# Optimization experiments

Measured on AMD Instinct MI355X. Metric: run time of the kernel, lower is better.

The kernel has to match this reference:

```python
import jax, jax.numpy as jnp
import numpy as np

V = 6          # num_variables
K = 6          # codebook_size
D = 32         # embedding_dim
C = 3          # channels
B = 64         # batch
N = K ** V     # 46656 codebook combinations
EPS = 1e-5     # torch BatchNorm eps
ENTROPY_SCALE = 0.1


def setup_inputs() -> dict:
    key = jax.random.key(0)
    ks = jax.random.split(key, 40)
    i = iter(range(40))
    def rn(shape, s):
        return jax.random.normal(ks[next(i)], shape, dtype=jnp.float32) * s
    def rv(shape):
        return 0.5 + 0.5 * jax.random.uniform(ks[next(i)], shape, dtype=jnp.float32)
    inp = {
        'x': jax.random.normal(ks[next(i)], (B, C, 7, 7), dtype=jnp.float32),
        # encoder
        'conv_w': rn((256, C, 7, 7), 0.08), 'conv_b': rn((256,), 0.01),
        'ebn2_g': 1.0 + rn((256,), 0.1), 'ebn2_b': rn((256,), 0.1),
        'fc1_w': rn((1024, 256), 0.06), 'fc1_b': rn((1024,), 0.01),
        'ebn1_g': 1.0 + rn((1024,), 0.1), 'ebn1_b': rn((1024,), 0.1),
        'fc2_w': rn((V * K, 1024), 0.03), 'fc2_b': rn((V * K,), 0.01),
        # quantizer embeddings (V separate codebooks)
        'embeds': jax.random.normal(ks[next(i)], (V, K, D), dtype=jnp.float32),
        # decoder
        'dfc1_w': rn((1024, V * D), 0.07), 'dfc1_b': rn((1024,), 0.01),
        'dbn1_g': 1.0 + rn((1024,), 0.1), 'dbn1_b': rn((1024,), 0.1),
        'dbn1_rm': rn((1024,), 0.1), 'dbn1_rv': rv((1024,)),
        'dfc2_w': rn((256, 1024), 0.03), 'dfc2_b': rn((256,), 0.01),
        'dbn2_g': 1.0 + rn((256,), 0.1), 'dbn2_b': rn((256,), 0.1),
        'dbn2_rm': rn((256,), 0.1), 'dbn2_rv': rv((256,)),
        'dct1_w': rn((256, 16, 7, 7), 0.05), 'dct1_b': rn((16,), 0.01),
        'dbn3_g': 1.0 + rn((16,), 0.1), 'dbn3_b': rn((16,), 0.1),
        'dbn3_rm': rn((16,), 0.1), 'dbn3_rv': rv((16,)),
        'dct2_w': rn((16, C), 0.2), 'dct2_b': rn((C,), 0.01),
    }
    return inp


def _bn_eval(t, g, b, rm, rvar):
    # eval-mode BatchNorm (running stats); params broadcast over leading dims
    return g * (t - rm) * jax.lax.rsqrt(rvar + EPS) + b


def _bn_train(t, g, b):
    # train-mode BatchNorm1d on (B, F): biased batch statistics over dim 0
    m = t.mean(0)
    v = ((t - m) ** 2).mean(0)
    return g * (t - m) * jax.lax.rsqrt(v + EPS) + b


def _decode_all(embeds, dfc1_w, dfc1_b, dbn1_g, dbn1_b, dbn1_rm, dbn1_rv,
                dfc2_w, dfc2_b, dbn2_g, dbn2_b, dbn2_rm, dbn2_rv,
                dct1_w, dct1_b, dbn3_g, dbn3_b, dbn3_rm, dbn3_rv,
                dct2_w, dct2_b):
    # enumerate all K^V index tuples in itertools.product order (first var slowest)
    idx = jnp.arange(N)
    powers = K ** (V - 1 - jnp.arange(V))
    combos = (idx[:, None] // powers[None, :]) % K          # (N, V)
    z = embeds[jnp.arange(V)[None, :], combos]              # (N, V, D) gather
    h = z.reshape(N, V * D) @ dfc1_w.T + dfc1_b             # (N, 1024)
    h = jax.nn.relu(_bn_eval(h, dbn1_g, dbn1_b, dbn1_rm, dbn1_rv))
    h = h @ dfc2_w.T + dfc2_b                               # (N, 256)
    h = jax.nn.relu(_bn_eval(h, dbn2_g, dbn2_b, dbn2_rm, dbn2_rv))
    # ConvTranspose2d(256,16,7,stride=2) on 1x1 input == einsum with full kernel
    h = jnp.einsum('ni,iohw->nohw', h, dct1_w) + dct1_b[:, None, None]  # (N,16,7,7)
    h = jax.nn.relu(_bn_eval(h, dbn3_g[:, None, None], dbn3_b[:, None, None],
                             dbn3_rm[:, None, None], dbn3_rv[:, None, None]))
    # ConvTranspose2d(16,C,1,1) == pointwise channel mix
    em = jnp.einsum('nihw,io->nohw', h, dct2_w) + dct2_b[:, None, None]  # (N,C,7,7)
    return em


def reference(x, conv_w, conv_b, ebn2_g, ebn2_b, fc1_w, fc1_b, ebn1_g, ebn1_b,
              fc2_w, fc2_b, embeds, dfc1_w, dfc1_b, dbn1_g, dbn1_b, dbn1_rm,
              dbn1_rv, dfc2_w, dfc2_b, dbn2_g, dbn2_b, dbn2_rm, dbn2_rv,
              dct1_w, dct1_b, dbn3_g, dbn3_b, dbn3_rm, dbn3_rv, dct2_w, dct2_b):
    # emission means for every codebook combination (batched decode, BN eval)
    em = _decode_all(embeds, dfc1_w, dfc1_b, dbn1_g, dbn1_b, dbn1_rm, dbn1_rv,
                     dfc2_w, dfc2_b, dbn2_g, dbn2_b, dbn2_rm, dbn2_rv,
                     dct1_w, dct1_b, dbn3_g, dbn3_b, dbn3_rm, dbn3_rv,
                     dct2_w, dct2_b)                         # (N, C, 7, 7)
    # encoder: Conv2d(C,256,7) on 7x7 input collapses to a single GEMM
    e = jnp.einsum('bchw,ochw->bo', x, conv_w) + conv_b      # (B, 256)
    e = jax.nn.relu(_bn_train(e, ebn2_g, ebn2_b))
    e = e @ fc1_w.T + fc1_b                                  # (B, 1024)
    e = jax.nn.relu(_bn_train(e, ebn1_g, ebn1_b))
    logits = e @ fc2_w.T + fc2_b                             # (B, V*K)
    # quantizer
    latent_dist = jax.nn.softmax(logits.reshape(B, V, K), axis=-1)
    latent_loss = ENTROPY_SCALE * jnp.sum(
        latent_dist * jnp.log(latent_dist + 1e-10), axis=(1, 2))
    # obs logits: -0.5 * ||em - x||^2 summed over (C,H,W), via expanded form
    E = em.reshape(N, -1)                                    # (N, 147)
    X = x.reshape(B, -1)                                     # (B, 147)
    obs = -0.5 * (jnp.sum(E * E, -1)[None, :]
                  - 2.0 * (X @ E.T)
                  + jnp.sum(X * X, -1)[:, None])             # (B, N)
    obs_logits = obs.reshape((B,) + (K,) * V)
    return obs_logits, latent_dist, latent_loss
```

## Files before the change

### kernel.cpp

```cpp
#include <hip/hip_runtime.h>
#include <math.h>

#define EPSF 1e-5f
#define NNC 46656

typedef __attribute__((ext_vector_type(4))) float  f32x4;
typedef __attribute__((ext_vector_type(8))) short  short8;
typedef __attribute__((ext_vector_type(8))) unsigned short ushort8;
typedef __attribute__((ext_vector_type(4))) unsigned int uint4v;

__device__ __forceinline__ float bf2f(unsigned short u) {
    unsigned int x = ((unsigned int)u) << 16;
    return __builtin_bit_cast(float, x);
}
__device__ __forceinline__ unsigned short f2bf(float f) {
    unsigned int x = __builtin_bit_cast(unsigned int, f);
    unsigned int r = (x + 0x7fffu + ((x >> 16) & 1u)) >> 16;
    return (unsigned short)r;
}

__device__ __forceinline__ short8 packrelu8(ushort8 H8, ushort8 S8) {
    uint4v H = __builtin_bit_cast(uint4v, H8);
    uint4v S = __builtin_bit_cast(uint4v, S8);
    uint4v O;
#pragma unroll
    for (int d = 0; d < 4; ++d) {
        float hlo = __builtin_bit_cast(float, H[d] << 16);
        float hhi = __builtin_bit_cast(float, H[d] & 0xffff0000u);
        float slo = __builtin_bit_cast(float, S[d] << 16);
        float shi = __builtin_bit_cast(float, S[d] & 0xffff0000u);
        unsigned int rlo = __builtin_bit_cast(unsigned int, fmaxf(hlo + slo, 0.f));
        unsigned int rhi = __builtin_bit_cast(unsigned int, fmaxf(hhi + shi, 0.f));
        O[d] = __builtin_amdgcn_perm(rhi, rlo, 0x07060302u);
    }
    return __builtin_bit_cast(short8, O);
}

#define WS_PP    0u
#define WS_C1    36864u
#define WS_SH    37888u
#define WS_S3    148480u
#define WS_W2BF  259072u
#define WS_C2    390144u
#define WS_W3BF  390400u
#define WS_C3    490752u
#define WS_XBF   490768u
#define WS_SX2   495888u
#define WS_E1T   495952u
#define WS_E2T   512336u

#define OBS_SIZE (64*NNC)
#define DIST_OFF OBS_SIZE
#define LOSS_OFF (OBS_SIZE + 64*36)

#define LDS_BYTES 75008


__global__ void dvae_k1(const float* __restrict__ x,
                        const float* __restrict__ conv_w, const float* __restrict__ conv_b,
                        const float* __restrict__ ebn2_g, const float* __restrict__ ebn2_b,
                        const float* __restrict__ embeds, const float* __restrict__ dfc1_w,
                        const float* __restrict__ dfc1_b,
                        const float* __restrict__ dbn1_g, const float* __restrict__ dbn1_b,
                        const float* __restrict__ dbn1_rm, const float* __restrict__ dbn1_rv,
                        const float* __restrict__ dfc2_w, const float* __restrict__ dfc2_b,
                        const float* __restrict__ dbn2_g, const float* __restrict__ dbn2_b,
                        const float* __restrict__ dbn2_rm, const float* __restrict__ dbn2_rv,
                        const float* __restrict__ dct1_w, const float* __restrict__ dct1_b,
                        const float* __restrict__ dbn3_g, const float* __restrict__ dbn3_b,
                        const float* __restrict__ dbn3_rm, const float* __restrict__ dbn3_rv,
                        float* __restrict__ ws) {
    __shared__ float sbuf[13504];
    int bx = blockIdx.x, tid = threadIdx.x;
    if (bx < 16) {
        float* wtile = sbuf;
        float* semb  = sbuf + 12352;
        int j0 = bx * 64;
        for (int e = tid; e < 64 * 192; e += 256)
            wtile[(e / 192) * 193 + (e % 192)] = dfc1_w[j0 * 192 + e];
        for (int e = tid; e < 1152; e += 256) semb[e] = embeds[e];
        __syncthreads();
        int jL = tid & 63, wvP = tid >> 6;
        int j = j0 + jL;
        float s1 = dbn1_g[j] * rsqrtf(dbn1_rv[j] + EPSF);
#pragma unroll
        for (int vkL = 0; vkL < 9; ++vkL) {
            int vk = wvP * 9 + vkL;
            int v = vk / 6;
            const float* wrow = &wtile[jL * 193 + v * 32];
            const float* ep = &semb[vk * 32];
            float dot = 0.f;
#pragma unroll
            for (int d = 0; d < 32; ++d) dot += wrow[d] * ep[d];
            ws[WS_PP + vk * 1024 + j] = s1 * dot;
        }
        if (tid < 64) {
            int jj = j0 + tid;
            float s = dbn1_g[jj] * rsqrtf(dbn1_rv[jj] + EPSF);
            ws[WS_C1 + jj] = s * dfc1_b[jj] + dbn1_b[jj] - dbn1_rm[jj] * s;
        }
    } else if (bx < 272) {
        int t = (bx - 16) * 256 + tid;
        int i = t >> 8, kq = (t & 255) * 4;
        float s2 = dbn2_g[i] * rsqrtf(dbn2_rv[i] + EPSF);
        float4 w = *(const float4*)(dfc2_w + i * 1024 + kq);
        unsigned short* dst = (unsigned short*)(ws + WS_W2BF) + i * 1024 + kq;
        dst[0] = f2bf(s2 * w.x); dst[1] = f2bf(s2 * w.y);
        dst[2] = f2bf(s2 * w.z); dst[3] = f2bf(s2 * w.w);
        if (kq == 0) ws[WS_C2 + i] = s2 * dfc2_b[i] + dbn2_b[i] - dbn2_rm[i] * s2;
    } else if (bx < 288) {
        int blk = bx - 272;
        for (int e = tid; e < 12544; e += 256) sbuf[e] = dct1_w[blk * 12544 + e];
        __syncthreads();
        unsigned short* W3 = (unsigned short*)(ws + WS_W3BF);
        for (int e = tid; e < 1568; e += 256) {
            int up = e >> 1, k8 = (e & 1) * 8;
            int o = up & 15, hw = up >> 4;
            float s3 = dbn3_g[o] * rsqrtf(dbn3_rv[o] + EPSF);
            ushort8 ov;
#pragma unroll
            for (int t = 0; t < 8; ++t)
                ov[t] = f2bf(s3 * sbuf[(k8 + t) * 784 + o * 49 + hw]);
            *(ushort8*)(W3 + up * 256 + blk * 16 + k8) = ov;
        }
        if (blk == 0 && tid < 16) {
            float s = dbn3_g[tid] * rsqrtf(dbn3_rv[tid] + EPSF);
            ws[WS_C3 + tid] = s * dct1_b[tid] + dbn3_b[tid] - dbn3_rm[tid] * s;
        }
    } else if (bx == 288) {
        unsigned short* Xb = (unsigned short*)(ws + WS_XBF);
        if (tid < 64) {
            const float* xp = x + tid * 147;
            float s = 0.f;
            for (int qq = 0; qq < 147; ++qq) { float v = xp[qq]; s += v * v; }
            ws[WS_SX2 + tid] = s;
        }
        for (int e = tid; e < 64 * 160; e += 256) {
            int b = e / 160, col = e % 160;
            float v = 0.f;
            if (col < 147) { int hw = col / 3, c = col % 3; v = x[b * 147 + c * 49 + hw]; }
            Xb[e] = f2bf(v);
        }
    } else {
        int blk = bx - 289;
        for (int e = tid; e < 9408; e += 256) sbuf[e] = x[e];
        __syncthreads();
        int b = tid & 63;
        int oL = __builtin_amdgcn_readfirstlane(tid >> 6);
        int o = blk * 4 + oL;
        const float* wp = conv_w + o * 147;
        float acc = conv_b[o];
        for (int qq = 0; qq < 147; ++qq) acc += sbuf[b * 147 + qq] * wp[qq];
        float m = acc;
#pragma unroll
        for (int s = 1; s < 64; s <<= 1) m += __shfl_xor(m, s);
        m *= (1.f / 64.f);
        float d = acc - m;
        float var = d * d;
#pragma unroll
        for (int s = 1; s < 64; s <<= 1) var += __shfl_xor(var, s);
        var *= (1.f / 64.f);
        float y = ebn2_g[o] * d * rsqrtf(var + EPSF) + ebn2_b[o];
        ws[WS_E1T + o * 64 + b] = fmaxf(y, 0.f);
    }
}


__global__ void dvae_k2(const float* __restrict__ fc1_w, const float* __restrict__ fc1_b,
                        const float* __restrict__ ebn1_g, const float* __restrict__ ebn1_b,
                        float* __restrict__ ws) {
    int bx = blockIdx.x, tid = threadIdx.x;
    const float* Pp = ws + WS_PP;
    if (bx < 108) {
        int t = bx * 256 + tid;
        int gh = t >> 7, kg = (t & 127) * 8;
        int d0 = gh / 36, d1 = (gh / 6) % 6, d2 = gh % 6;
        const float* r0 = Pp + d0 * 1024 + kg;
        const float* r1 = Pp + (6 + d1) * 1024 + kg;
        const float* r2 = Pp + (12 + d2) * 1024 + kg;
        const float* cc = ws + WS_C1 + kg;
        ushort8 o;
#pragma unroll
        for (int e = 0; e < 8; ++e) o[e] = f2bf(cc[e] + r0[e] + r1[e] + r2[e]);
        *(ushort8*)((unsigned short*)(ws + WS_SH) + gh * 1024 + kg) = o;
    } else if (bx < 216) {
        int t = (bx - 108) * 256 + tid;
        int gl = t >> 7, kg = (t & 127) * 8;
        int d3 = gl / 36, d4 = (gl / 6) % 6, d5 = gl % 6;
        const float* r3 = Pp + (18 + d3) * 1024 + kg;
        const float* r4 = Pp + (24 + d4) * 1024 + kg;
        const float* r5 = Pp + (30 + d5) * 1024 + kg;
        ushort8 o;
#pragma unroll
        for (int e = 0; e < 8; ++e) o[e] = f2bf(r3[e] + r4[e] + r5[e]);
        *(ushort8*)((unsigned short*)(ws + WS_S3) + gl * 1024 + kg) = o;
    } else {
        int blk = bx - 216;
        int b = tid & 63;
        int jL = __builtin_amdgcn_readfirstlane(tid >> 6);
        int j = blk * 4 + jL;
        const float* e1 = ws + WS_E1T;
        const float* wp = fc1_w + j * 256;
        float acc = fc1_b[j];
        for (int o = 0; o < 256; ++o) acc += e1[o * 64 + b] * wp[o];
        float m = acc;
#pragma unroll
        for (int s = 1; s < 64; s <<= 1) m += __shfl_xor(m, s);
        m *= (1.f / 64.f);
        float d = acc - m;
        float var = d * d;
#pragma unroll
        for (int s = 1; s < 64; s <<= 1) var += __shfl_xor(var, s);
        var *= (1.f / 64.f);
        float y = ebn1_g[j] * d * rsqrtf(var + EPSF) + ebn1_b[j];
        ws[WS_E2T + j * 64 + b] = fmaxf(y, 0.f);
    }
}


__launch_bounds__(256, 2)
__global__ void dvae_k3(const unsigned short* __restrict__ Sh,
                        const unsigned short* __restrict__ S3g,
                        const unsigned short* __restrict__ W2,
                        const float* __restrict__ c2g,
                        const unsigned short* __restrict__ W3,
                        const float* __restrict__ c3g,
                        const float* __restrict__ d2wg,
                        const float* __restrict__ d2bg,
                        const unsigned short* __restrict__ Xg,
                        const float* __restrict__ sx2g,
                        const float* __restrict__ e2T,
                        const float* __restrict__ fc2_w,
                        const float* __restrict__ fc2_b,
                        float* __restrict__ out) {
    extern __shared__ char sm[];
    int tid = threadIdx.x;

    if (blockIdx.x == 0) {
        float* wch = (float*)sm;
        float* ech = (float*)(sm + 18432);
        float* LG  = (float*)(sm + 51200);
        int b = tid & 63;
        int wvU = __builtin_amdgcn_readfirstlane(tid >> 6);
        float accv[9];
#pragma unroll
        for (int it = 0; it < 9; ++it) accv[it] = 0.f;
        for (int ch = 0; ch < 8; ++ch) {
            __syncthreads();
            for (int e = tid; e < 36 * 128; e += 256) {
                int o = e >> 7, jl = e & 127;
                wch[e] = fc2_w[o * 1024 + ch * 128 + jl];
            }
            for (int e = tid; e < 128 * 64; e += 256)
                ech[e] = e2T[(ch * 128 + (e >> 6)) * 64 + (e & 63)];
            __syncthreads();
            for (int jl = 0; jl < 128; ++jl) {
                float ev = ech[jl * 64 + b];
#pragma unroll
                for (int it = 0; it < 9; ++it)
                    accv[it] += ev * wch[(wvU + it * 4) * 128 + jl];
            }
        }
#pragma unroll
        for (int it = 0; it < 9; ++it) {
            int o = wvU + it * 4;
            LG[b * 36 + o] = accv[it] + fc2_b[o];
        }
        __syncthreads();
        if (tid < 64) {
            float loss = 0.f;
#pragma unroll
            for (int v = 0; v < 6; ++v) {
                float mx = -1e30f;
#pragma unroll
                for (int k = 0; k < 6; ++k) mx = fmaxf(mx, LG[tid * 36 + v * 6 + k]);
                float s = 0.f, ex[6];
#pragma unroll
                for (int k = 0; k < 6; ++k) { ex[k] = expf(LG[tid * 36 + v * 6 + k] - mx); s += ex[k]; }
                float inv = 1.f / s;
#pragma unroll
                for (int k = 0; k < 6; ++k) {
                    float dd = ex[k] * inv;
                    out[DIST_OFF + tid * 36 + v * 6 + k] = dd;
                    loss += dd * logf(dd + 1e-10f);
                }
            }
            out[LOSS_OFF + tid] = 0.1f * loss;
        }
        return;
    }

    int wv = tid >> 6, lane = tid & 63, l15 = lane & 15, q = lane >> 4;
    int nbase = (blockIdx.x - 1) * 64;
    float* sE2p = (float*)(sm + 0);
    float* sE2f = (float*)(sm + 1024);
    unsigned short* emL = (unsigned short*)(sm + 1280);
    float* h3w = (float*)(sm + 21760 + wv * 5120);
    unsigned short* h2L = (unsigned short*)(sm + 42240);

    f32x4 acc[4][4];
#pragma unroll
    for (int a = 0; a < 4; ++a)
#pragma unroll
        for (int b = 0; b < 4; ++b) acc[a][b] = (f32x4){0.f, 0.f, 0.f, 0.f};

    const unsigned short* pSh[4];
    const unsigned short* pS3[4];
#pragma unroll
    for (int mt = 0; mt < 4; ++mt) {
        int nm = nbase + mt * 16 + l15;
        int gh = nm / 216;
        int r216 = nm - gh * 216;
        pSh[mt] = Sh + gh * 1024 + q * 8;
        pS3[mt] = S3g + r216 * 1024 + q * 8;
    }
    const unsigned short* bbase = W2 + (wv * 64 + l15) * 1024 + q * 8;

    ushort8 sa[4], sb[4];
    short8 bpre[4];
#pragma unroll
    for (int mt = 0; mt < 4; ++mt) { sa[mt] = *(const ushort8*)(pSh[mt]); sb[mt] = *(const ushort8*)(pS3[mt]); }
#pragma unroll
    for (int j = 0; j < 4; ++j) bpre[j] = *(const short8*)(bbase + j * 16384);

#pragma unroll 2
    for (int s = 0; s < 32; ++s) {
        short8 af[4];
#pragma unroll
        for (int mt = 0; mt < 4; ++mt) af[mt] = packrelu8(sa[mt], sb[mt]);
        short8 bcur[4];
#pragma unroll
        for (int j = 0; j < 4; ++j) bcur[j] = bpre[j];
        if (s < 31) {
            int off = (s + 1) * 32;
#pragma unroll
            for (int mt = 0; mt < 4; ++mt) {
                sa[mt] = *(const ushort8*)(pSh[mt] + off);
                sb[mt] = *(const ushort8*)(pS3[mt] + off);
            }
#pragma unroll
            for (int j = 0; j < 4; ++j) bpre[j] = *(const short8*)(bbase + j * 16384 + off);
        }
#pragma unroll
        for (int mt = 0; mt < 4; ++mt)
#pragma unroll
            for (int j = 0; j < 4; ++j)
                acc[mt][j] = __builtin_amdgcn_mfma_f32_16x16x32_bf16(af[mt], bcur[j], acc[mt][j], 0, 0, 0);
    }
#pragma unroll
    for (int j = 0; j < 4; ++j) {
        int i = wv * 64 + j * 16 + l15;
        float cc = c2g[i];
#pragma unroll
        for (int mt = 0; mt < 4; ++mt)
#pragma unroll
            for (int r = 0; r < 4; ++r) {
                int m = mt * 16 + q * 4 + r;
                h2L[((i >> 3) * 64 + m) * 8 + (i & 7)] = f2bf(fmaxf(acc[mt][j][r] + cc, 0.f));
            }
    }
    __syncthreads();

    float c3v = c3g[l15];
    float db0 = d2bg[0], db1 = d2bg[1], db2 = d2bg[2];
    float dw0[16], dw1[16], dw2[16];
#pragma unroll
    for (int o = 0; o < 16; ++o) {
        dw0[o] = d2wg[o * 3 + 0]; dw1[o] = d2wg[o * 3 + 1]; dw2[o] = d2wg[o * 3 + 2];
    }
    float sE2a = 0.f;
    for (int c = wv; c < 13; c += 4) {
        int hw0 = c * 4;
        f32x4 a2[4][4];
#pragma unroll
        for (int a = 0; a < 4; ++a)
#pragma unroll
            for (int b = 0; b < 4; ++b) a2[a][b] = (f32x4){0.f, 0.f, 0.f, 0.f};
        const unsigned short* b3[4];
#pragma unroll
        for (int j = 0; j < 4; ++j) {
            int hw = hw0 + j; if (hw > 48) hw = 48;
            b3[j] = W3 + (hw * 16 + l15) * 256 + q * 8;
        }
        short8 bpre2[4];
#pragma unroll
        for (int j = 0; j < 4; ++j) bpre2[j] = *(const short8*)(b3[j]);
#pragma unroll
        for (int s = 0; s < 8; ++s) {
            short8 bcur[4];
#pragma unroll
            for (int j = 0; j < 4; ++j) bcur[j] = bpre2[j];
            if (s < 7) {
#pragma unroll
                for (int j = 0; j < 4; ++j) bpre2[j] = *(const short8*)(b3[j] + (s + 1) * 32);
            }
            short8 af[4];
#pragma unroll
            for (int mt = 0; mt < 4; ++mt)
                af[mt] = *(const short8*)(h2L + ((s * 4 + q) * 64 + mt * 16 + l15) * 8);
#pragma unroll
            for (int mt = 0; mt < 4; ++mt)
#pragma unroll
                for (int j = 0; j < 4; ++j)
                    a2[mt][j] = __builtin_amdgcn_mfma_f32_16x16x32_bf16(af[mt], bcur[j], a2[mt][j], 0, 0, 0);
        }
#pragma unroll
        for (int j = 0; j < 4; ++j) {
            int hw = hw0 + j;
            if (hw <= 48) {
#pragma unroll
                for (int mt = 0; mt < 4; ++mt)
#pragma unroll
                    for (int r = 0; r < 4; ++r)
                        h3w[(mt * 16 + q * 4 + r) * 20 + l15] = fmaxf(a2[mt][j][r] + c3v, 0.f);
                float hvv[16];
#pragma unroll
                for (int g = 0; g < 4; ++g) {
                    f32x4 tv = *(const f32x4*)(h3w + lane * 20 + g * 4);
                    hvv[g * 4 + 0] = tv[0]; hvv[g * 4 + 1] = tv[1];
                    hvv[g * 4 + 2] = tv[2]; hvv[g * 4 + 3] = tv[3];
                }
                float e0 = db0, e1 = db1, e2 = db2;
#pragma unroll
                for (int o = 0; o < 16; ++o) {
                    e0 += hvv[o] * dw0[o]; e1 += hvv[o] * dw1[o]; e2 += hvv[o] * dw2[o];
                }
                unsigned short u0 = f2bf(e0), u1 = f2bf(e1), u2 = f2bf(e2);
                float f0 = bf2f(u0), f1 = bf2f(u1), f2v = bf2f(u2);
                sE2a += f0 * f0 + f1 * f1 + f2v * f2v;
                emL[lane * 160 + hw * 3 + 0] = u0;
                emL[lane * 160 + hw * 3 + 1] = u1;
                emL[lane * 160 + hw * 3 + 2] = u2;
            }
        }
    }
    sE2p[wv * 64 + lane] = sE2a;
    for (int e = tid; e < 64 * 13; e += 256) emL[(e / 13) * 160 + 147 + (e % 13)] = 0;
    __syncthreads();
    if (tid < 64) sE2f[tid] = sE2p[tid] + sE2p[64 + tid] + sE2p[128 + tid] + sE2p[192 + tid];
    __syncthreads();

    f32x4 aO[4];
#pragma unroll
    for (int j = 0; j < 4; ++j) aO[j] = (f32x4){0.f, 0.f, 0.f, 0.f};
    const unsigned short* xrow = Xg + (wv * 16 + l15) * 160 + q * 8;
#pragma unroll
    for (int s = 0; s < 5; ++s) {
        short8 af = *(const short8*)(xrow + s * 32);
#pragma unroll
        for (int j = 0; j < 4; ++j) {
            short8 bfv = *(const short8*)(emL + (j * 16 + l15) * 160 + s * 32 + q * 8);
            aO[j] = __builtin_amdgcn_mfma_f32_16x16x32_bf16(af, bfv, aO[j], 0, 0, 0);
        }
    }
    int b0 = wv * 16 + q * 4;
    float sxv[4];
#pragma unroll
    for (int r = 0; r < 4; ++r) sxv[r] = sx2g[b0 + r];
#pragma unroll
    for (int j = 0; j < 4; ++j) {
        int n = nbase + j * 16 + l15;
        float he = 0.5f * sE2f[j * 16 + l15];
#pragma unroll
        for (int r = 0; r < 4; ++r)
            out[(size_t)(b0 + r) * NNC + n] = aO[j][r] - he - 0.5f * sxv[r];
    }
}


extern "C" void kernel_launch(void* const* d_in, const int* in_sizes, int n_in,
                              void* d_out, int out_size, void* d_ws, size_t ws_size,
                              hipStream_t stream) {
    const float* x       = (const float*)d_in[0];
    const float* conv_w  = (const float*)d_in[1];
    const float* conv_b  = (const float*)d_in[2];
    const float* ebn2_g  = (const float*)d_in[3];
    const float* ebn2_b  = (const float*)d_in[4];
    const float* fc1_w   = (const float*)d_in[5];
    const float* fc1_b   = (const float*)d_in[6];
    const float* ebn1_g  = (const float*)d_in[7];
    const float* ebn1_b  = (const float*)d_in[8];
    const float* fc2_w   = (const float*)d_in[9];
    const float* fc2_b   = (const float*)d_in[10];
    const float* embeds  = (const float*)d_in[11];
    const float* dfc1_w  = (const float*)d_in[12];
    const float* dfc1_b  = (const float*)d_in[13];
    const float* dbn1_g  = (const float*)d_in[14];
    const float* dbn1_b  = (const float*)d_in[15];
    const float* dbn1_rm = (const float*)d_in[16];
    const float* dbn1_rv = (const float*)d_in[17];
    const float* dfc2_w  = (const float*)d_in[18];
    const float* dfc2_b  = (const float*)d_in[19];
    const float* dbn2_g  = (const float*)d_in[20];
    const float* dbn2_b  = (const float*)d_in[21];
    const float* dbn2_rm = (const float*)d_in[22];
    const float* dbn2_rv = (const float*)d_in[23];
    const float* dct1_w  = (const float*)d_in[24];
    const float* dct1_b  = (const float*)d_in[25];
    const float* dbn3_g  = (const float*)d_in[26];
    const float* dbn3_b  = (const float*)d_in[27];
    const float* dbn3_rm = (const float*)d_in[28];
    const float* dbn3_rv = (const float*)d_in[29];
    const float* dct2_w  = (const float*)d_in[30];
    const float* dct2_b  = (const float*)d_in[31];

    float* ws  = (float*)d_ws;
    float* out = (float*)d_out;

    dvae_k1<<<353, 256, 0, stream>>>(x, conv_w, conv_b, ebn2_g, ebn2_b,
                                     embeds, dfc1_w, dfc1_b, dbn1_g, dbn1_b, dbn1_rm, dbn1_rv,
                                     dfc2_w, dfc2_b, dbn2_g, dbn2_b, dbn2_rm, dbn2_rv,
                                     dct1_w, dct1_b, dbn3_g, dbn3_b, dbn3_rm, dbn3_rv, ws);
    dvae_k2<<<472, 256, 0, stream>>>(fc1_w, fc1_b, ebn1_g, ebn1_b, ws);

    hipFuncSetAttribute(reinterpret_cast<const void*>(dvae_k3),
                        hipFuncAttributeMaxDynamicSharedMemorySize, LDS_BYTES);
    dvae_k3<<<730, 256, LDS_BYTES, stream>>>(
        (const unsigned short*)(ws + WS_SH), (const unsigned short*)(ws + WS_S3),
        (const unsigned short*)(ws + WS_W2BF), ws + WS_C2,
        (const unsigned short*)(ws + WS_W3BF), ws + WS_C3,
        dct2_w, dct2_b,
        (const unsigned short*)(ws + WS_XBF), ws + WS_SX2,
        ws + WS_E2T, fc2_w, fc2_b, out);
}
```

Before: 279.1 us.

## Halve k3 codebook tile to 32 rows to raise occupancy and block count

The main decoder/obs kernel now processes 32 codebook combinations per block instead of 64. This halves LDS use and accumulator registers, raises launch bounds to 4 blocks per SIMD set, and doubles the grid to about 1459 blocks for better latency hiding and load balance. In exchange, the fc2 weight B-fragments are reused over fewer rows, so W2/W3 global loads per output double, and half the lanes sit idle in the decode epilogue. The first kernel's dfc1 projection is also split across 64 smaller blocks, and two scalar loops get unroll pragmas.

```diff
diff --git a/kernel.cpp b/kernel.cpp
--- a/kernel.cpp
+++ b/kernel.cpp
@@ -53,7 +53,7 @@
 #define DIST_OFF OBS_SIZE
 #define LOSS_OFF (OBS_SIZE + 64*36)
 
-#define LDS_BYTES 75008
+#define LDS_BYTES 37504
 
 
 __global__ void dvae_k1(const float* __restrict__ x,
@@ -70,22 +70,20 @@
                         const float* __restrict__ dbn3_g, const float* __restrict__ dbn3_b,
                         const float* __restrict__ dbn3_rm, const float* __restrict__ dbn3_rv,
                         float* __restrict__ ws) {
-    __shared__ float sbuf[13504];
+    __shared__ float sbuf[12544];
     int bx = blockIdx.x, tid = threadIdx.x;
-    if (bx < 16) {
+    if (bx < 64) {
         float* wtile = sbuf;
-        float* semb  = sbuf + 12352;
-        int j0 = bx * 64;
-        for (int e = tid; e < 64 * 192; e += 256)
+        float* semb  = sbuf + 3088;
+        int j0 = bx * 16;
+        for (int e = tid; e < 16 * 192; e += 256)
             wtile[(e / 192) * 193 + (e % 192)] = dfc1_w[j0 * 192 + e];
         for (int e = tid; e < 1152; e += 256) semb[e] = embeds[e];
         __syncthreads();
-        int jL = tid & 63, wvP = tid >> 6;
+        int jL = tid & 15, vk0 = tid >> 4;
         int j = j0 + jL;
         float s1 = dbn1_g[j] * rsqrtf(dbn1_rv[j] + EPSF);
-#pragma unroll
-        for (int vkL = 0; vkL < 9; ++vkL) {
-            int vk = wvP * 9 + vkL;
+        for (int vk = vk0; vk < 36; vk += 16) {
             int v = vk / 6;
             const float* wrow = &wtile[jL * 193 + v * 32];
             const float* ep = &semb[vk * 32];
@@ -94,13 +92,13 @@
             for (int d = 0; d < 32; ++d) dot += wrow[d] * ep[d];
             ws[WS_PP + vk * 1024 + j] = s1 * dot;
         }
-        if (tid < 64) {
+        if (tid < 16) {
             int jj = j0 + tid;
             float s = dbn1_g[jj] * rsqrtf(dbn1_rv[jj] + EPSF);
             ws[WS_C1 + jj] = s * dfc1_b[jj] + dbn1_b[jj] - dbn1_rm[jj] * s;
         }
-    } else if (bx < 272) {
-        int t = (bx - 16) * 256 + tid;
+    } else if (bx < 320) {
+        int t = (bx - 64) * 256 + tid;
         int i = t >> 8, kq = (t & 255) * 4;
         float s2 = dbn2_g[i] * rsqrtf(dbn2_rv[i] + EPSF);
         float4 w = *(const float4*)(dfc2_w + i * 1024 + kq);
@@ -108,8 +106,8 @@
         dst[0] = f2bf(s2 * w.x); dst[1] = f2bf(s2 * w.y);
         dst[2] = f2bf(s2 * w.z); dst[3] = f2bf(s2 * w.w);
         if (kq == 0) ws[WS_C2 + i] = s2 * dfc2_b[i] + dbn2_b[i] - dbn2_rm[i] * s2;
-    } else if (bx < 288) {
-        int blk = bx - 272;
+    } else if (bx < 336) {
+        int blk = bx - 320;
         for (int e = tid; e < 12544; e += 256) sbuf[e] = dct1_w[blk * 12544 + e];
         __syncthreads();
         unsigned short* W3 = (unsigned short*)(ws + WS_W3BF);
@@ -119,15 +117,15 @@
             float s3 = dbn3_g[o] * rsqrtf(dbn3_rv[o] + EPSF);
             ushort8 ov;
 #pragma unroll
-            for (int t = 0; t < 8; ++t)
-                ov[t] = f2bf(s3 * sbuf[(k8 + t) * 784 + o * 49 + hw]);
+            for (int t2 = 0; t2 < 8; ++t2)
+                ov[t2] = f2bf(s3 * sbuf[(k8 + t2) * 784 + o * 49 + hw]);
             *(ushort8*)(W3 + up * 256 + blk * 16 + k8) = ov;
         }
         if (blk == 0 && tid < 16) {
             float s = dbn3_g[tid] * rsqrtf(dbn3_rv[tid] + EPSF);
             ws[WS_C3 + tid] = s * dct1_b[tid] + dbn3_b[tid] - dbn3_rm[tid] * s;
         }
-    } else if (bx == 288) {
+    } else if (bx == 336) {
         unsigned short* Xb = (unsigned short*)(ws + WS_XBF);
         if (tid < 64) {
             const float* xp = x + tid * 147;
@@ -142,7 +140,7 @@
             Xb[e] = f2bf(v);
         }
     } else {
-        int blk = bx - 289;
+        int blk = bx - 337;
         for (int e = tid; e < 9408; e += 256) sbuf[e] = x[e];
         __syncthreads();
         int b = tid & 63;
@@ -150,6 +148,7 @@
         int o = blk * 4 + oL;
         const float* wp = conv_w + o * 147;
         float acc = conv_b[o];
+#pragma unroll 7
         for (int qq = 0; qq < 147; ++qq) acc += sbuf[b * 147 + qq] * wp[qq];
         float m = acc;
 #pragma unroll
@@ -202,6 +201,7 @@
         const float* e1 = ws + WS_E1T;
         const float* wp = fc1_w + j * 256;
         float acc = fc1_b[j];
+#pragma unroll 8
         for (int o = 0; o < 256; ++o) acc += e1[o * 64 + b] * wp[o];
         float m = acc;
 #pragma unroll
@@ -218,7 +218,7 @@
 }
 
 
-__launch_bounds__(256, 2)
+__launch_bounds__(256, 4)
 __global__ void dvae_k3(const unsigned short* __restrict__ Sh,
                         const unsigned short* __restrict__ S3g,
                         const unsigned short* __restrict__ W2,
@@ -238,27 +238,25 @@
 
     if (blockIdx.x == 0) {
         float* wch = (float*)sm;
-        float* ech = (float*)(sm + 18432);
-        float* LG  = (float*)(sm + 51200);
+        float* ech = (float*)(sm + 9216);
+        float* LG  = (float*)(sm + 25600);
         int b = tid & 63;
         int wvU = __builtin_amdgcn_readfirstlane(tid >> 6);
         float accv[9];
 #pragma unroll
         for (int it = 0; it < 9; ++it) accv[it] = 0.f;
-        for (int ch = 0; ch < 8; ++ch) {
+        for (int ch = 0; ch < 16; ++ch) {
             __syncthreads();
-            for (int e = tid; e < 36 * 128; e += 256) {
-                int o = e >> 7, jl = e & 127;
-                wch[e] = fc2_w[o * 1024 + ch * 128 + jl];
-            }
-            for (int e = tid; e < 128 * 64; e += 256)
-                ech[e] = e2T[(ch * 128 + (e >> 6)) * 64 + (e & 63)];
+            for (int e = tid; e < 36 * 64; e += 256)
+                wch[e] = fc2_w[(e >> 6) * 1024 + ch * 64 + (e & 63)];
+            for (int e = tid; e < 64 * 64; e += 256)
+                ech[e] = e2T[(ch * 64 + (e >> 6)) * 64 + (e & 63)];
             __syncthreads();
-            for (int jl = 0; jl < 128; ++jl) {
+            for (int jl = 0; jl < 64; ++jl) {
                 float ev = ech[jl * 64 + b];
 #pragma unroll
                 for (int it = 0; it < 9; ++it)
-                    accv[it] += ev * wch[(wvU + it * 4) * 128 + jl];
+                    accv[it] += ev * wch[(wvU + it * 4) * 64 + jl];
             }
         }
 #pragma unroll
@@ -291,23 +289,23 @@
     }
 
     int wv = tid >> 6, lane = tid & 63, l15 = lane & 15, q = lane >> 4;
-    int nbase = (blockIdx.x - 1) * 64;
+    int nbase = (blockIdx.x - 1) * 32;
     float* sE2p = (float*)(sm + 0);
-    float* sE2f = (float*)(sm + 1024);
-    unsigned short* emL = (unsigned short*)(sm + 1280);
-    float* h3w = (float*)(sm + 21760 + wv * 5120);
-    unsigned short* h2L = (unsigned short*)(sm + 42240);
-
-    f32x4 acc[4][4];
-#pragma unroll
-    for (int a = 0; a < 4; ++a)
+    float* sE2f = (float*)(sm + 512);
+    unsigned short* emL = (unsigned short*)(sm + 640);
+    float* h3w = (float*)(sm + 10880 + wv * 2560);
+    unsigned short* h2L = (unsigned short*)(sm + 21120);
+
+    f32x4 acc[2][4];
+#pragma unroll
+    for (int a = 0; a < 2; ++a)
 #pragma unroll
         for (int b = 0; b < 4; ++b) acc[a][b] = (f32x4){0.f, 0.f, 0.f, 0.f};
 
-    const unsigned short* pSh[4];
-    const unsigned short* pS3[4];
-#pragma unroll
-    for (int mt = 0; mt < 4; ++mt) {
+    const unsigned short* pSh[2];
+    const unsigned short* pS3[2];
+#pragma unroll
+    for (int mt = 0; mt < 2; ++mt) {
         int nm = nbase + mt * 16 + l15;
         int gh = nm / 216;
         int r216 = nm - gh * 216;
@@ -316,25 +314,25 @@
     }
     const unsigned short* bbase = W2 + (wv * 64 + l15) * 1024 + q * 8;
 
-    ushort8 sa[4], sb[4];
+    ushort8 sa[2], sb[2];
     short8 bpre[4];
 #pragma unroll
-    for (int mt = 0; mt < 4; ++mt) { sa[mt] = *(const ushort8*)(pSh[mt]); sb[mt] = *(const ushort8*)(pS3[mt]); }
+    for (int mt = 0; mt < 2; ++mt) { sa[mt] = *(const ushort8*)(pSh[mt]); sb[mt] = *(const ushort8*)(pS3[mt]); }
 #pragma unroll
     for (int j = 0; j < 4; ++j) bpre[j] = *(const short8*)(bbase + j * 16384);
 
 #pragma unroll 2
     for (int s = 0; s < 32; ++s) {
-        short8 af[4];
-#pragma unroll
-        for (int mt = 0; mt < 4; ++mt) af[mt] = packrelu8(sa[mt], sb[mt]);
+        short8 af[2];
+#pragma unroll
+        for (int mt = 0; mt < 2; ++mt) af[mt] = packrelu8(sa[mt], sb[mt]);
         short8 bcur[4];
 #pragma unroll
         for (int j = 0; j < 4; ++j) bcur[j] = bpre[j];
         if (s < 31) {
             int off = (s + 1) * 32;
 #pragma unroll
-            for (int mt = 0; mt < 4; ++mt) {
+            for (int mt = 0; mt < 2; ++mt) {
                 sa[mt] = *(const ushort8*)(pSh[mt] + off);
                 sb[mt] = *(const ushort8*)(pS3[mt] + off);
             }
@@ -342,7 +340,7 @@
             for (int j = 0; j < 4; ++j) bpre[j] = *(const short8*)(bbase + j * 16384 + off);
         }
 #pragma unroll
-        for (int mt = 0; mt < 4; ++mt)
+        for (int mt = 0; mt < 2; ++mt)
 #pragma unroll
             for (int j = 0; j < 4; ++j)
                 acc[mt][j] = __builtin_amdgcn_mfma_f32_16x16x32_bf16(af[mt], bcur[j], acc[mt][j], 0, 0, 0);
@@ -352,11 +350,11 @@
         int i = wv * 64 + j * 16 + l15;
         float cc = c2g[i];
 #pragma unroll
-        for (int mt = 0; mt < 4; ++mt)
+        for (int mt = 0; mt < 2; ++mt)
 #pragma unroll
             for (int r = 0; r < 4; ++r) {
                 int m = mt * 16 + q * 4 + r;
-                h2L[((i >> 3) * 64 + m) * 8 + (i & 7)] = f2bf(fmaxf(acc[mt][j][r] + cc, 0.f));
+                h2L[((i >> 3) * 32 + m) * 8 + (i & 7)] = f2bf(fmaxf(acc[mt][j][r] + cc, 0.f));
             }
     }
     __syncthreads();
@@ -371,9 +369,9 @@
     float sE2a = 0.f;
     for (int c = wv; c < 13; c += 4) {
         int hw0 = c * 4;
-        f32x4 a2[4][4];
-#pragma unroll
-        for (int a = 0; a < 4; ++a)
+        f32x4 a2[2][4];
+#pragma unroll
+        for (int a = 0; a < 2; ++a)
 #pragma unroll
             for (int b = 0; b < 4; ++b) a2[a][b] = (f32x4){0.f, 0.f, 0.f, 0.f};
         const unsigned short* b3[4];
@@ -394,12 +392,12 @@
 #pragma unroll
                 for (int j = 0; j < 4; ++j) bpre2[j] = *(const short8*)(b3[j] + (s + 1) * 32);
             }
-            short8 af[4];
-#pragma unroll
-            for (int mt = 0; mt < 4; ++mt)
-                af[mt] = *(const short8*)(h2L + ((s * 4 + q) * 64 + mt * 16 + l15) * 8);
-#pragma unroll
-            for (int mt = 0; mt < 4; ++mt)
+            short8 af[2];
+#pragma unroll
+            for (int mt = 0; mt < 2; ++mt)
+                af[mt] = *(const short8*)(h2L + ((s * 4 + q) * 32 + mt * 16 + l15) * 8);
+#pragma unroll
+            for (int mt = 0; mt < 2; ++mt)
 #pragma unroll
                 for (int j = 0; j < 4; ++j)
                     a2[mt][j] = __builtin_amdgcn_mfma_f32_16x16x32_bf16(af[mt], bcur[j], a2[mt][j], 0, 0, 0);
@@ -409,46 +407,49 @@
             int hw = hw0 + j;
             if (hw <= 48) {
 #pragma unroll
-                for (int mt = 0; mt < 4; ++mt)
+                for (int mt = 0; mt < 2; ++mt)
 #pragma unroll
                     for (int r = 0; r < 4; ++r)
                         h3w[(mt * 16 + q * 4 + r) * 20 + l15] = fmaxf(a2[mt][j][r] + c3v, 0.f);
-                float hvv[16];
-#pragma unroll
-                for (int g = 0; g < 4; ++g) {
-                    f32x4 tv = *(const f32x4*)(h3w + lane * 20 + g * 4);
-                    hvv[g * 4 + 0] = tv[0]; hvv[g * 4 + 1] = tv[1];
-                    hvv[g * 4 + 2] = tv[2]; hvv[g * 4 + 3] = tv[3];
+                if (lane < 32) {
+                    int m = lane;
+                    float hvv[16];
+#pragma unroll
+                    for (int g = 0; g < 4; ++g) {
+                        f32x4 tv = *(const f32x4*)(h3w + m * 20 + g * 4);
+                        hvv[g * 4 + 0] = tv[0]; hvv[g * 4 + 1] = tv[1];
+                        hvv[g * 4 + 2] = tv[2]; hvv[g * 4 + 3] = tv[3];
+                    }
+                    float e0 = db0, e1 = db1, e2 = db2;
+#pragma unroll
+                    for (int o = 0; o < 16; ++o) {
+                        e0 += hvv[o] * dw0[o]; e1 += hvv[o] * dw1[o]; e2 += hvv[o] * dw2[o];
+                    }
+                    unsigned short u0 = f2bf(e0), u1 = f2bf(e1), u2 = f2bf(e2);
+                    float f0 = bf2f(u0), f1 = bf2f(u1), f2v = bf2f(u2);
+                    sE2a += f0 * f0 + f1 * f1 + f2v * f2v;
+                    emL[m * 160 + hw * 3 + 0] = u0;
+                    emL[m * 160 + hw * 3 + 1] = u1;
+                    emL[m * 160 + hw * 3 + 2] = u2;
                 }
-                float e0 = db0, e1 = db1, e2 = db2;
-#pragma unroll
-                for (int o = 0; o < 16; ++o) {
-                    e0 += hvv[o] * dw0[o]; e1 += hvv[o] * dw1[o]; e2 += hvv[o] * dw2[o];
-                }
-                unsigned short u0 = f2bf(e0), u1 = f2bf(e1), u2 = f2bf(e2);
-                float f0 = bf2f(u0), f1 = bf2f(u1), f2v = bf2f(u2);
-                sE2a += f0 * f0 + f1 * f1 + f2v * f2v;
-                emL[lane * 160 + hw * 3 + 0] = u0;
-                emL[lane * 160 + hw * 3 + 1] = u1;
-                emL[lane * 160 + hw * 3 + 2] = u2;
             }
         }
     }
-    sE2p[wv * 64 + lane] = sE2a;
-    for (int e = tid; e < 64 * 13; e += 256) emL[(e / 13) * 160 + 147 + (e % 13)] = 0;
+    if (lane < 32) sE2p[wv * 32 + lane] = sE2a;
+    for (int e = tid; e < 32 * 13; e += 256) emL[(e / 13) * 160 + 147 + (e % 13)] = 0;
     __syncthreads();
-    if (tid < 64) sE2f[tid] = sE2p[tid] + sE2p[64 + tid] + sE2p[128 + tid] + sE2p[192 + tid];
+    if (tid < 32) sE2f[tid] = sE2p[tid] + sE2p[32 + tid] + sE2p[64 + tid] + sE2p[96 + tid];
     __syncthreads();
 
-    f32x4 aO[4];
-#pragma unroll
-    for (int j = 0; j < 4; ++j) aO[j] = (f32x4){0.f, 0.f, 0.f, 0.f};
+    f32x4 aO[2];
+#pragma unroll
+    for (int j = 0; j < 2; ++j) aO[j] = (f32x4){0.f, 0.f, 0.f, 0.f};
     const unsigned short* xrow = Xg + (wv * 16 + l15) * 160 + q * 8;
 #pragma unroll
     for (int s = 0; s < 5; ++s) {
         short8 af = *(const short8*)(xrow + s * 32);
 #pragma unroll
-        for (int j = 0; j < 4; ++j) {
+        for (int j = 0; j < 2; ++j) {
             short8 bfv = *(const short8*)(emL + (j * 16 + l15) * 160 + s * 32 + q * 8);
             aO[j] = __builtin_amdgcn_mfma_f32_16x16x32_bf16(af, bfv, aO[j], 0, 0, 0);
         }
@@ -458,7 +459,7 @@
 #pragma unroll
     for (int r = 0; r < 4; ++r) sxv[r] = sx2g[b0 + r];
 #pragma unroll
-    for (int j = 0; j < 4; ++j) {
+    for (int j = 0; j < 2; ++j) {
         int n = nbase + j * 16 + l15;
         float he = 0.5f * sE2f[j * 16 + l15];
 #pragma unroll
@@ -507,15 +508,13 @@
     float* ws  = (float*)d_ws;
     float* out = (float*)d_out;
 
-    dvae_k1<<<353, 256, 0, stream>>>(x, conv_w, conv_b, ebn2_g, ebn2_b,
+    dvae_k1<<<401, 256, 0, stream>>>(x, conv_w, conv_b, ebn2_g, ebn2_b,
                                      embeds, dfc1_w, dfc1_b, dbn1_g, dbn1_b, dbn1_rm, dbn1_rv,
                                      dfc2_w, dfc2_b, dbn2_g, dbn2_b, dbn2_rm, dbn2_rv,
                                      dct1_w, dct1_b, dbn3_g, dbn3_b, dbn3_rm, dbn3_rv, ws);
     dvae_k2<<<472, 256, 0, stream>>>(fc1_w, fc1_b, ebn1_g, ebn1_b, ws);
 
-    hipFuncSetAttribute(reinterpret_cast<const void*>(dvae_k3),
-                        hipFuncAttributeMaxDynamicSharedMemorySize, LDS_BYTES);
-    dvae_k3<<<730, 256, LDS_BYTES, stream>>>(
+    dvae_k3<<<NNC / 32 + 1, 256, LDS_BYTES, stream>>>(
         (const unsigned short*)(ws + WS_SH), (const unsigned short*)(ws + WS_S3),
         (const unsigned short*)(ws + WS_W2BF), ws + WS_C2,
         (const unsigned short*)(ws + WS_W3BF), ws + WS_C3,
```

Result: slower. 375.1 us (+34.4%).

## Eliminate middle kernel: fold Sh/S3 build into k1, fc1 into k3 with flag

Applied to the files above, without the earlier changes.

Drops the second kernel launch. The Sh/S3 bf16 table construction moves into the first kernel's projection blocks, which now cover 16 output columns each and write the tables directly instead of staging partial products in the workspace. The fc1+BatchNorm encoder layer moves into 256 extra blocks of the third kernel, and the logits block spin-waits on an atomic counter until they finish. This saves one launch and one workspace round trip, but it relies on the fc1 blocks being scheduled before or alongside the waiting block, and it adds 256 small blocks to the main kernel.

```diff
diff --git a/kernel.cpp b/kernel.cpp
--- a/kernel.cpp
+++ b/kernel.cpp
@@ -36,8 +36,6 @@
     return __builtin_bit_cast(short8, O);
 }
 
-#define WS_PP    0u
-#define WS_C1    36864u
 #define WS_SH    37888u
 #define WS_S3    148480u
 #define WS_W2BF  259072u
@@ -48,6 +46,7 @@
 #define WS_SX2   495888u
 #define WS_E1T   495952u
 #define WS_E2T   512336u
+#define WS_FLAG  577872u
 
 #define OBS_SIZE (64*NNC)
 #define DIST_OFF OBS_SIZE
@@ -70,37 +69,48 @@
                         const float* __restrict__ dbn3_g, const float* __restrict__ dbn3_b,
                         const float* __restrict__ dbn3_rm, const float* __restrict__ dbn3_rv,
                         float* __restrict__ ws) {
-    __shared__ float sbuf[13504];
+    __shared__ float sbuf[12544];
     int bx = blockIdx.x, tid = threadIdx.x;
-    if (bx < 16) {
+    if (bx < 64) {
         float* wtile = sbuf;
-        float* semb  = sbuf + 12352;
-        int j0 = bx * 64;
-        for (int e = tid; e < 64 * 192; e += 256)
+        float* semb  = sbuf + 3088;
+        float* Pt    = sbuf + 4240;
+        float* c1s   = sbuf + 4960;
+        int j0 = bx * 16;
+        for (int e = tid; e < 16 * 192; e += 256)
             wtile[(e / 192) * 193 + (e % 192)] = dfc1_w[j0 * 192 + e];
         for (int e = tid; e < 1152; e += 256) semb[e] = embeds[e];
         __syncthreads();
-        int jL = tid & 63, wvP = tid >> 6;
-        int j = j0 + jL;
-        float s1 = dbn1_g[j] * rsqrtf(dbn1_rv[j] + EPSF);
-#pragma unroll
-        for (int vkL = 0; vkL < 9; ++vkL) {
-            int vk = wvP * 9 + vkL;
+        for (int e = tid; e < 576; e += 256) {
+            int vk = e >> 4, jL = e & 15;
             int v = vk / 6;
+            int j = j0 + jL;
             const float* wrow = &wtile[jL * 193 + v * 32];
             const float* ep = &semb[vk * 32];
             float dot = 0.f;
 #pragma unroll
             for (int d = 0; d < 32; ++d) dot += wrow[d] * ep[d];
-            ws[WS_PP + vk * 1024 + j] = s1 * dot;
-        }
-        if (tid < 64) {
-            int jj = j0 + tid;
-            float s = dbn1_g[jj] * rsqrtf(dbn1_rv[jj] + EPSF);
-            ws[WS_C1 + jj] = s * dfc1_b[jj] + dbn1_b[jj] - dbn1_rm[jj] * s;
-        }
-    } else if (bx < 272) {
-        int t = (bx - 16) * 256 + tid;
+            float s1 = dbn1_g[j] * rsqrtf(dbn1_rv[j] + EPSF);
+            Pt[vk * 20 + jL] = s1 * dot;
+        }
+        if (tid < 16) {
+            int j = j0 + tid;
+            float s = dbn1_g[j] * rsqrtf(dbn1_rv[j] + EPSF);
+            c1s[tid] = s * dfc1_b[j] + dbn1_b[j] - dbn1_rm[j] * s;
+        }
+        __syncthreads();
+        unsigned short* Sh = (unsigned short*)(ws + WS_SH);
+        unsigned short* S3 = (unsigned short*)(ws + WS_S3);
+        for (int e = tid; e < 216 * 16; e += 256) {
+            int gh = e >> 4, jL = e & 15;
+            int d0 = gh / 36, d1 = (gh / 6) % 6, d2 = gh % 6;
+            float vh = c1s[jL] + Pt[d0 * 20 + jL] + Pt[(6 + d1) * 20 + jL] + Pt[(12 + d2) * 20 + jL];
+            float vs = Pt[(18 + d0) * 20 + jL] + Pt[(24 + d1) * 20 + jL] + Pt[(30 + d2) * 20 + jL];
+            Sh[gh * 1024 + j0 + jL] = f2bf(vh);
+            S3[gh * 1024 + j0 + jL] = f2bf(vs);
+        }
+    } else if (bx < 320) {
+        int t = (bx - 64) * 256 + tid;
         int i = t >> 8, kq = (t & 255) * 4;
         float s2 = dbn2_g[i] * rsqrtf(dbn2_rv[i] + EPSF);
         float4 w = *(const float4*)(dfc2_w + i * 1024 + kq);
@@ -108,8 +118,8 @@
         dst[0] = f2bf(s2 * w.x); dst[1] = f2bf(s2 * w.y);
         dst[2] = f2bf(s2 * w.z); dst[3] = f2bf(s2 * w.w);
         if (kq == 0) ws[WS_C2 + i] = s2 * dfc2_b[i] + dbn2_b[i] - dbn2_rm[i] * s2;
-    } else if (bx < 288) {
-        int blk = bx - 272;
+    } else if (bx < 336) {
+        int blk = bx - 320;
         for (int e = tid; e < 12544; e += 256) sbuf[e] = dct1_w[blk * 12544 + e];
         __syncthreads();
         unsigned short* W3 = (unsigned short*)(ws + WS_W3BF);
@@ -119,16 +129,17 @@
             float s3 = dbn3_g[o] * rsqrtf(dbn3_rv[o] + EPSF);
             ushort8 ov;
 #pragma unroll
-            for (int t = 0; t < 8; ++t)
-                ov[t] = f2bf(s3 * sbuf[(k8 + t) * 784 + o * 49 + hw]);
+            for (int t2 = 0; t2 < 8; ++t2)
+                ov[t2] = f2bf(s3 * sbuf[(k8 + t2) * 784 + o * 49 + hw]);
             *(ushort8*)(W3 + up * 256 + blk * 16 + k8) = ov;
         }
         if (blk == 0 && tid < 16) {
             float s = dbn3_g[tid] * rsqrtf(dbn3_rv[tid] + EPSF);
             ws[WS_C3 + tid] = s * dct1_b[tid] + dbn3_b[tid] - dbn3_rm[tid] * s;
         }
-    } else if (bx == 288) {
+    } else if (bx == 336) {
         unsigned short* Xb = (unsigned short*)(ws + WS_XBF);
+        if (tid == 0) *(int*)(ws + WS_FLAG) = 0;
         if (tid < 64) {
             const float* xp = x + tid * 147;
             float s = 0.f;
@@ -142,7 +153,7 @@
             Xb[e] = f2bf(v);
         }
     } else {
-        int blk = bx - 289;
+        int blk = bx - 337;
         for (int e = tid; e < 9408; e += 256) sbuf[e] = x[e];
         __syncthreads();
         int b = tid & 63;
@@ -150,6 +161,7 @@
         int o = blk * 4 + oL;
         const float* wp = conv_w + o * 147;
         float acc = conv_b[o];
+#pragma unroll 7
         for (int qq = 0; qq < 147; ++qq) acc += sbuf[b * 147 + qq] * wp[qq];
         float m = acc;
 #pragma unroll
@@ -162,58 +174,6 @@
         var *= (1.f / 64.f);
         float y = ebn2_g[o] * d * rsqrtf(var + EPSF) + ebn2_b[o];
         ws[WS_E1T + o * 64 + b] = fmaxf(y, 0.f);
-    }
-}
-
-
-__global__ void dvae_k2(const float* __restrict__ fc1_w, const float* __restrict__ fc1_b,
-                        const float* __restrict__ ebn1_g, const float* __restrict__ ebn1_b,
-                        float* __restrict__ ws) {
-    int bx = blockIdx.x, tid = threadIdx.x;
-    const float* Pp = ws + WS_PP;
-    if (bx < 108) {
-        int t = bx * 256 + tid;
-        int gh = t >> 7, kg = (t & 127) * 8;
-        int d0 = gh / 36, d1 = (gh / 6) % 6, d2 = gh % 6;
-        const float* r0 = Pp + d0 * 1024 + kg;
-        const float* r1 = Pp + (6 + d1) * 1024 + kg;
-        const float* r2 = Pp + (12 + d2) * 1024 + kg;
-        const float* cc = ws + WS_C1 + kg;
-        ushort8 o;
-#pragma unroll
-        for (int e = 0; e < 8; ++e) o[e] = f2bf(cc[e] + r0[e] + r1[e] + r2[e]);
-        *(ushort8*)((unsigned short*)(ws + WS_SH) + gh * 1024 + kg) = o;
-    } else if (bx < 216) {
-        int t = (bx - 108) * 256 + tid;
-        int gl = t >> 7, kg = (t & 127) * 8;
-        int d3 = gl / 36, d4 = (gl / 6) % 6, d5 = gl % 6;
-        const float* r3 = Pp + (18 + d3) * 1024 + kg;
-        const float* r4 = Pp + (24 + d4) * 1024 + kg;
-        const float* r5 = Pp + (30 + d5) * 1024 + kg;
-        ushort8 o;
-#pragma unroll
-        for (int e = 0; e < 8; ++e) o[e] = f2bf(r3[e] + r4[e] + r5[e]);
-        *(ushort8*)((unsigned short*)(ws + WS_S3) + gl * 1024 + kg) = o;
-    } else {
-        int blk = bx - 216;
-        int b = tid & 63;
-        int jL = __builtin_amdgcn_readfirstlane(tid >> 6);
-        int j = blk * 4 + jL;
-        const float* e1 = ws + WS_E1T;
-        const float* wp = fc1_w + j * 256;
-        float acc = fc1_b[j];
-        for (int o = 0; o < 256; ++o) acc += e1[o * 64 + b] * wp[o];
-        float m = acc;
-#pragma unroll
-        for (int s = 1; s < 64; s <<= 1) m += __shfl_xor(m, s);
-        m *= (1.f / 64.f);
-        float d = acc - m;
-        float var = d * d;
-#pragma unroll
-        for (int s = 1; s < 64; s <<= 1) var += __shfl_xor(var, s);
-        var *= (1.f / 64.f);
-        float y = ebn1_g[j] * d * rsqrtf(var + EPSF) + ebn1_b[j];
-        ws[WS_E2T + j * 64 + b] = fmaxf(y, 0.f);
     }
 }
 
@@ -229,14 +189,47 @@
                         const float* __restrict__ d2bg,
                         const unsigned short* __restrict__ Xg,
                         const float* __restrict__ sx2g,
-                        const float* __restrict__ e2T,
+                        const float* __restrict__ fc1_w, const float* __restrict__ fc1_b,
+                        const float* __restrict__ ebn1_g, const float* __restrict__ ebn1_b,
+                        const float* __restrict__ e1T,
+                        float* __restrict__ e2T,
+                        int* __restrict__ flag,
                         const float* __restrict__ fc2_w,
                         const float* __restrict__ fc2_b,
                         float* __restrict__ out) {
     extern __shared__ char sm[];
     int tid = threadIdx.x;
 
-    if (blockIdx.x == 0) {
+    if (blockIdx.x < 256) {
+        int blk = blockIdx.x;
+        int b = tid & 63;
+        int jL = __builtin_amdgcn_readfirstlane(tid >> 6);
+        int j = blk * 4 + jL;
+        const float* wp = fc1_w + j * 256;
+        float acc = fc1_b[j];
+#pragma unroll 8
+        for (int o = 0; o < 256; ++o) acc += e1T[o * 64 + b] * wp[o];
+        float m = acc;
+#pragma unroll
+        for (int s = 1; s < 64; s <<= 1) m += __shfl_xor(m, s);
+        m *= (1.f / 64.f);
+        float d = acc - m;
+        float var = d * d;
+#pragma unroll
+        for (int s = 1; s < 64; s <<= 1) var += __shfl_xor(var, s);
+        var *= (1.f / 64.f);
+        float y = ebn1_g[j] * d * rsqrtf(var + EPSF) + ebn1_b[j];
+        e2T[j * 64 + b] = fmaxf(y, 0.f);
+        __syncthreads();
+        if (tid == 0) { __threadfence(); atomicAdd(flag, 1); }
+        return;
+    }
+
+    if (blockIdx.x == 256) {
+        if (tid == 0) {
+            while (atomicAdd(flag, 0) < 256) __builtin_amdgcn_s_sleep(8);
+        }
+        __syncthreads();
         float* wch = (float*)sm;
         float* ech = (float*)(sm + 18432);
         float* LG  = (float*)(sm + 51200);
@@ -247,10 +240,8 @@
         for (int it = 0; it < 9; ++it) accv[it] = 0.f;
         for (int ch = 0; ch < 8; ++ch) {
             __syncthreads();
-            for (int e = tid; e < 36 * 128; e += 256) {
-                int o = e >> 7, jl = e & 127;
-                wch[e] = fc2_w[o * 1024 + ch * 128 + jl];
-            }
+            for (int e = tid; e < 36 * 128; e += 256)
+                wch[e] = fc2_w[(e >> 7) * 1024 + ch * 128 + (e & 127)];
             for (int e = tid; e < 128 * 64; e += 256)
                 ech[e] = e2T[(ch * 128 + (e >> 6)) * 64 + (e & 63)];
             __syncthreads();
@@ -291,7 +282,7 @@
     }
 
     int wv = tid >> 6, lane = tid & 63, l15 = lane & 15, q = lane >> 4;
-    int nbase = (blockIdx.x - 1) * 64;
+    int nbase = (blockIdx.x - 257) * 64;
     float* sE2p = (float*)(sm + 0);
     float* sE2f = (float*)(sm + 1024);
     unsigned short* emL = (unsigned short*)(sm + 1280);
@@ -507,19 +498,20 @@
     float* ws  = (float*)d_ws;
     float* out = (float*)d_out;
 
-    dvae_k1<<<353, 256, 0, stream>>>(x, conv_w, conv_b, ebn2_g, ebn2_b,
+    dvae_k1<<<401, 256, 0, stream>>>(x, conv_w, conv_b, ebn2_g, ebn2_b,
                                      embeds, dfc1_w, dfc1_b, dbn1_g, dbn1_b, dbn1_rm, dbn1_rv,
                                      dfc2_w, dfc2_b, dbn2_g, dbn2_b, dbn2_rm, dbn2_rv,
                                      dct1_w, dct1_b, dbn3_g, dbn3_b, dbn3_rm, dbn3_rv, ws);
-    dvae_k2<<<472, 256, 0, stream>>>(fc1_w, fc1_b, ebn1_g, ebn1_b, ws);
 
     hipFuncSetAttribute(reinterpret_cast<const void*>(dvae_k3),
                         hipFuncAttributeMaxDynamicSharedMemorySize, LDS_BYTES);
-    dvae_k3<<<730, 256, LDS_BYTES, stream>>>(
+    dvae_k3<<<986, 256, LDS_BYTES, stream>>>(
         (const unsigned short*)(ws + WS_SH), (const unsigned short*)(ws + WS_S3),
         (const unsigned short*)(ws + WS_W2BF), ws + WS_C2,
         (const unsigned short*)(ws + WS_W3BF), ws + WS_C3,
         dct2_w, dct2_b,
         (const unsigned short*)(ws + WS_XBF), ws + WS_SX2,
-        ws + WS_E2T, fc2_w, fc2_b, out);
+        fc1_w, fc1_b, ebn1_g, ebn1_b,
+        ws + WS_E1T, ws + WS_E2T, (int*)(ws + WS_FLAG),
+        fc2_w, fc2_b, out);
 }
```

Measured after the change: 274.0 us. About the same (-1.8%).
